# Performance work log

Measured on AMD Instinct MI355X. Metric: run time of the kernel, lower is better.

Reference implementation:

```python
import jax, jax.numpy as jnp
import numpy as np

GROUP_SIZE = 128


def setup_inputs() -> dict:
    key = jax.random.key(0)
    k1, k2, k3 = jax.random.split(key, 3)
    B, S, IN, OUT = 4, 8192, 1024, 1024
    x = jax.random.normal(k1, (B, S, IN), dtype=jnp.float32)
    weight = jax.random.normal(k2, (OUT, IN), dtype=jnp.float32) * 0.02
    bias = jax.random.normal(k3, (OUT,), dtype=jnp.float32) * 0.01
    return {"x": x, "weight": weight, "bias": bias}


def reference(x, weight, bias):
    """Quantized int8 path: quantize() + _forward_int8 of OneBitLinear.

    - weights binarized to +/-1 int8 (sign, with 0 -> -1, matching
      sign().clamp(min=0) bit packing then 2*bit-1)
    - per-group weight scales = group absmax, stored fp16 (as in quantize())
    - activations dynamically quantized per-token to int8
    - int32-accumulated GEMM, rescaled by x_scale * mean group scale per row
    """
    out_f, in_f = weight.shape
    ng = in_f // GROUP_SIZE
    w_g = weight.reshape(out_f, ng, GROUP_SIZE)
    # per-group absmax scales, cast fp16 -> fp32 to mimic fp16 storage
    scales = jnp.maximum(jnp.max(jnp.abs(w_g), axis=-1), 1e-8)
    scales = scales.astype(jnp.float16).astype(jnp.float32)  # [O, ng]
    # +/-1 int8 weights (sign>0 -> +1, else -1; zero maps to -1 like the packer)
    w_int8 = jnp.where(weight > 0, 1, -1).astype(jnp.int8)  # [O, I]

    # dynamic per-token activation quantization
    x_f = x.reshape(-1, in_f)  # [BT, I]
    x_scale = jnp.maximum(jnp.max(jnp.abs(x_f), axis=1, keepdims=True), 1e-8) / 127.0
    x_int8 = jnp.clip(jnp.round(x_f / x_scale), -128, 127).astype(jnp.int8)

    # int8 GEMM with int32 accumulation
    out_i32 = jnp.matmul(
        x_int8.astype(jnp.int32), w_int8.T.astype(jnp.int32)
    )  # [BT, O]

    w_scale_per_row = jnp.mean(scales, axis=1)  # [O]
    out_f32 = out_i32.astype(jnp.float32) * x_scale * w_scale_per_row[None, :]
    out_f32 = out_f32 + bias[None, :]
    return out_f32.reshape(*x.shape[:-1], out_f)
```

## Files before the change

kernel.cpp:

```cpp
#include <hip/hip_runtime.h>
#include <hip/hip_fp16.h>

#define K_DIM 1024
#define N_DIM 1024

typedef int v4i __attribute__((ext_vector_type(4)));

__device__ __forceinline__ void async_load16(const void* g, void* l) {
    __builtin_amdgcn_global_load_lds(
        (const __attribute__((address_space(1))) unsigned int*)g,
        (__attribute__((address_space(3))) unsigned int*)l,
        16, 0, 0);
}

#define BAR() do { asm volatile("" ::: "memory"); \
                   __builtin_amdgcn_s_barrier();  \
                   asm volatile("" ::: "memory"); } while (0)
#define VMCNT0() asm volatile("s_waitcnt vmcnt(0)" ::: "memory")

__global__ __launch_bounds__(256) void prep_w(const float* __restrict__ w,
                                              signed char* __restrict__ wq,
                                              float* __restrict__ wscale) {
    const int lane = threadIdx.x & 63;
    const int row  = blockIdx.x * 4 + (threadIdx.x >> 6);
    const float4* wr = (const float4*)(w + (size_t)row * K_DIM);
    float4 v[4];
#pragma unroll
    for (int j = 0; j < 4; ++j) v[j] = wr[lane * 4 + j];

    float g = 0.f;
#pragma unroll
    for (int j = 0; j < 4; ++j) {
        g = fmaxf(g, fabsf(v[j].x)); g = fmaxf(g, fabsf(v[j].y));
        g = fmaxf(g, fabsf(v[j].z)); g = fmaxf(g, fabsf(v[j].w));
    }
    g = fmaxf(g, __shfl_xor(g, 1, 64));
    g = fmaxf(g, __shfl_xor(g, 2, 64));
    g = fmaxf(g, __shfl_xor(g, 4, 64));
    const float s = __half2float(__float2half(fmaxf(g, 1e-8f)));
    float t = s;
    t += __shfl_xor(t, 8, 64);
    t += __shfl_xor(t, 16, 64);
    t += __shfl_xor(t, 32, 64);
    if (lane == 0) wscale[row] = t * 0.125f;

    int pk[4];
#pragma unroll
    for (int j = 0; j < 4; ++j) {
        const int b0 = (v[j].x > 0.f) ? 1 : -1;
        const int b1 = (v[j].y > 0.f) ? 1 : -1;
        const int b2 = (v[j].z > 0.f) ? 1 : -1;
        const int b3 = (v[j].w > 0.f) ? 1 : -1;
        pk[j] = (b0 & 255) | ((b1 & 255) << 8) | ((b2 & 255) << 16) | (b3 << 24);
    }
    *(int4*)(wq + (size_t)row * K_DIM + lane * 16) = make_int4(pk[0], pk[1], pk[2], pk[3]);
}

__global__ __launch_bounds__(256) void quant_x(const float* __restrict__ x,
                                               signed char* __restrict__ xq,
                                               float* __restrict__ xs) {
    const int lane = threadIdx.x & 63;
    const int row  = blockIdx.x * 4 + (threadIdx.x >> 6);
    const float4* xr = (const float4*)(x + (size_t)row * K_DIM);
    float4 v[4];
#pragma unroll
    for (int j = 0; j < 4; ++j) v[j] = xr[lane * 4 + j];

    float am = 0.f;
#pragma unroll
    for (int j = 0; j < 4; ++j) {
        am = fmaxf(am, fabsf(v[j].x)); am = fmaxf(am, fabsf(v[j].y));
        am = fmaxf(am, fabsf(v[j].z)); am = fmaxf(am, fabsf(v[j].w));
    }
#pragma unroll
    for (int off = 32; off >= 1; off >>= 1) am = fmaxf(am, __shfl_xor(am, off, 64));
    const float scale = fmaxf(am, 1e-8f) / 127.f;
    const float inv   = 1.0f / scale;

    int pk[4];
#pragma unroll
    for (int j = 0; j < 4; ++j) {
        const int b0 = (int)fminf(fmaxf(rintf(v[j].x * inv), -128.f), 127.f);
        const int b1 = (int)fminf(fmaxf(rintf(v[j].y * inv), -128.f), 127.f);
        const int b2 = (int)fminf(fmaxf(rintf(v[j].z * inv), -128.f), 127.f);
        const int b3 = (int)fminf(fmaxf(rintf(v[j].w * inv), -128.f), 127.f);
        pk[j] = (b0 & 255) | ((b1 & 255) << 8) | ((b2 & 255) << 16) | (b3 << 24);
    }
    *(int4*)(xq + (size_t)row * K_DIM + lane * 16) = make_int4(pk[0], pk[1], pk[2], pk[3]);
    if (lane == 0) xs[row] = scale;
}

__global__ __launch_bounds__(512, 2) void gemm_i8(const signed char* __restrict__ A,
                                                  const signed char* __restrict__ Bw,
                                                  const float* __restrict__ xs,
                                                  const float* __restrict__ wscale,
                                                  const float* __restrict__ bias,
                                                  float* __restrict__ out) {
    __shared__ __align__(16) signed char As[2][256 * 64];
    __shared__ __align__(16) signed char Bs[2][256 * 64];

    const int tid  = threadIdx.x;
    const int lane = tid & 63;
    const int wave = tid >> 6;
    const int wm   = wave >> 2;
    const int wn   = wave & 3;

    const int bid  = blockIdx.x;
    const int wgid = (bid & 7) * 64 + (bid >> 3);
    const int mT   = wgid >> 2;
    const int nT   = wgid & 3;
    const size_t mBase = (size_t)mT * 256;
    const int    nBase = nT * 256;

    const int srow = tid >> 2;
    const int skq  = (tid & 3) * 16;
    const signed char* Ag = A  + (mBase + srow) * K_DIM + skq;
    const signed char* Bg = Bw + (size_t)(nBase + srow) * K_DIM + skq;
    const int soff = tid * 16;

#define STAGE(b, kt) do {                                                   \
        const int _ko = (kt) * 64;                                          \
        async_load16(Ag + _ko,                         &As[b][soff]);       \
        async_load16(Ag + (size_t)128 * K_DIM + _ko,   &As[b][8192 + soff]);\
        async_load16(Bg + _ko,                         &Bs[b][soff]);       \
        async_load16(Bg + (size_t)128 * K_DIM + _ko,   &Bs[b][8192 + soff]);\
    } while (0)

    v4i acc[8][4] = {};

    const int r16 = lane & 15;
    const int g16 = (lane >> 4) * 16;
    const int aoff = (wm * 128 + r16) * 64 + g16;
    const int boff = (wn * 64  + r16) * 64 + g16;

    STAGE(0, 0);
    VMCNT0();
    BAR();

    for (int t = 0; t < 16; ++t) {
        const signed char* Ab = As[t & 1];
        const signed char* Bb = Bs[t & 1];

        if (t < 15) STAGE((t + 1) & 1, t + 1);

        v4i af[8], bf[4];
#pragma unroll
        for (int mf = 0; mf < 8; ++mf)
            af[mf] = *(const v4i*)(Ab + aoff + mf * (16 * 64));
#pragma unroll
        for (int nf = 0; nf < 4; ++nf)
            bf[nf] = *(const v4i*)(Bb + boff + nf * (16 * 64));

#pragma unroll
        for (int mf = 0; mf < 8; ++mf)
#pragma unroll
            for (int nf = 0; nf < 4; ++nf)
                acc[mf][nf] = __builtin_amdgcn_mfma_i32_16x16x64_i8(
                    af[mf], bf[nf], acc[mf][nf], 0, 0, 0);

        if (t < 15) {
            __builtin_amdgcn_sched_barrier(0);
            VMCNT0();
            BAR();
        }
    }
#undef STAGE

    const int cc = r16;
    const int rq = (lane >> 4) * 4;
    float xsr[8][4];
#pragma unroll
    for (int mf = 0; mf < 8; ++mf)
#pragma unroll
        for (int i = 0; i < 4; ++i)
            xsr[mf][i] = xs[mBase + wm * 128 + mf * 16 + rq + i];

#pragma unroll
    for (int nf = 0; nf < 4; ++nf) {
        const int col  = nBase + wn * 64 + nf * 16 + cc;
        const float wsc = wscale[col];
        const float bb  = bias[col];
#pragma unroll
        for (int mf = 0; mf < 8; ++mf) {
#pragma unroll
            for (int i = 0; i < 4; ++i) {
                const size_t row = mBase + wm * 128 + mf * 16 + rq + i;
                out[row * N_DIM + col] = (float)acc[mf][nf][i] * xsr[mf][i] * wsc + bb;
            }
        }
    }
}

extern "C" void kernel_launch(void* const* d_in, const int* in_sizes, int n_in,
                              void* d_out, int out_size, void* d_ws, size_t ws_size,
                              hipStream_t stream) {
    const float* x    = (const float*)d_in[0];
    const float* w    = (const float*)d_in[1];
    const float* bias = (const float*)d_in[2];
    float* out = (float*)d_out;

    const int BT = in_sizes[0] / K_DIM;

    char* ws = (char*)d_ws;
    signed char* xq     = (signed char*)ws;
    float*       xs     = (float*)(ws + (size_t)BT * K_DIM);
    signed char* wq     = (signed char*)(ws + (size_t)BT * K_DIM + (size_t)BT * 4);
    float*       wscale = (float*)((char*)wq + (size_t)N_DIM * K_DIM);

    prep_w<<<N_DIM / 4, 256, 0, stream>>>(w, wq, wscale);
    quant_x<<<BT / 4, 256, 0, stream>>>(x, xq, xs);
    gemm_i8<<<(BT / 256) * (N_DIM / 256), 512, 0, stream>>>(xq, wq, xs, wscale, bias, out);
}
```

Measured before the change: 303.5 us.

## Fuse activation quantization into GEMM with full-K int8 A tile in LDS

Removes the separate quant_x kernel. Each GEMM workgroup now quantizes its own 128 rows of x straight into a swizzled 128KB LDS buffer holding the full K extent, then sweeps all four 256-wide N tiles while streaming only B tiles through double-buffered LDS. This drops the int8 activation round trip through global memory and one kernel launch. In exchange it uses 160KB of dynamic LDS, which limits occupancy to one workgroup per CU. The grid shrinks to 256 workgroups, the quantization phase is not overlapped with MFMA work, and B is re-read from L2 by every workgroup.

```diff
diff --git a/kernel.cpp b/kernel.cpp
--- a/kernel.cpp
+++ b/kernel.cpp
@@ -56,136 +56,130 @@
     *(int4*)(wq + (size_t)row * K_DIM + lane * 16) = make_int4(pk[0], pk[1], pk[2], pk[3]);
 }
 
-__global__ __launch_bounds__(256) void quant_x(const float* __restrict__ x,
-                                               signed char* __restrict__ xq,
-                                               float* __restrict__ xs) {
-    const int lane = threadIdx.x & 63;
-    const int row  = blockIdx.x * 4 + (threadIdx.x >> 6);
-    const float4* xr = (const float4*)(x + (size_t)row * K_DIM);
-    float4 v[4];
-#pragma unroll
-    for (int j = 0; j < 4; ++j) v[j] = xr[lane * 4 + j];
-
-    float am = 0.f;
-#pragma unroll
-    for (int j = 0; j < 4; ++j) {
-        am = fmaxf(am, fabsf(v[j].x)); am = fmaxf(am, fabsf(v[j].y));
-        am = fmaxf(am, fabsf(v[j].z)); am = fmaxf(am, fabsf(v[j].w));
-    }
-#pragma unroll
-    for (int off = 32; off >= 1; off >>= 1) am = fmaxf(am, __shfl_xor(am, off, 64));
-    const float scale = fmaxf(am, 1e-8f) / 127.f;
-    const float inv   = 1.0f / scale;
-
-    int pk[4];
-#pragma unroll
-    for (int j = 0; j < 4; ++j) {
-        const int b0 = (int)fminf(fmaxf(rintf(v[j].x * inv), -128.f), 127.f);
-        const int b1 = (int)fminf(fmaxf(rintf(v[j].y * inv), -128.f), 127.f);
-        const int b2 = (int)fminf(fmaxf(rintf(v[j].z * inv), -128.f), 127.f);
-        const int b3 = (int)fminf(fmaxf(rintf(v[j].w * inv), -128.f), 127.f);
-        pk[j] = (b0 & 255) | ((b1 & 255) << 8) | ((b2 & 255) << 16) | (b3 << 24);
-    }
-    *(int4*)(xq + (size_t)row * K_DIM + lane * 16) = make_int4(pk[0], pk[1], pk[2], pk[3]);
-    if (lane == 0) xs[row] = scale;
-}
-
-__global__ __launch_bounds__(512, 2) void gemm_i8(const signed char* __restrict__ A,
-                                                  const signed char* __restrict__ Bw,
-                                                  const float* __restrict__ xs,
-                                                  const float* __restrict__ wscale,
-                                                  const float* __restrict__ bias,
-                                                  float* __restrict__ out) {
-    __shared__ __align__(16) signed char As[2][256 * 64];
-    __shared__ __align__(16) signed char Bs[2][256 * 64];
+__global__ __launch_bounds__(512, 2) void qgemm(const float* __restrict__ x,
+                                                const signed char* __restrict__ Bw,
+                                                const float* __restrict__ wscale,
+                                                const float* __restrict__ bias,
+                                                float* __restrict__ xsg,
+                                                float* __restrict__ out) {
+    extern __shared__ __align__(16) signed char smem[];
+    signed char* As = smem;
+    signed char* Bs = smem + 131072;
 
     const int tid  = threadIdx.x;
     const int lane = tid & 63;
     const int wave = tid >> 6;
-    const int wm   = wave >> 2;
-    const int wn   = wave & 3;
-
-    const int bid  = blockIdx.x;
-    const int wgid = (bid & 7) * 64 + (bid >> 3);
-    const int mT   = wgid >> 2;
-    const int nT   = wgid & 3;
-    const size_t mBase = (size_t)mT * 256;
-    const int    nBase = nT * 256;
+    const size_t mBase = (size_t)blockIdx.x * 128;
+
+    for (int rb = 0; rb < 4; ++rb) {
+        const int r0 = wave * 16 + rb * 4;
+        float4 v[4][4];
+#pragma unroll
+        for (int rr = 0; rr < 4; ++rr) {
+            const float4* xr = (const float4*)(x + (mBase + r0 + rr) * K_DIM);
+#pragma unroll
+            for (int j = 0; j < 4; ++j) v[rr][j] = xr[lane * 4 + j];
+        }
+#pragma unroll
+        for (int rr = 0; rr < 4; ++rr) {
+            const int r = r0 + rr;
+            float am = 0.f;
+#pragma unroll
+            for (int j = 0; j < 4; ++j) {
+                am = fmaxf(am, fabsf(v[rr][j].x)); am = fmaxf(am, fabsf(v[rr][j].y));
+                am = fmaxf(am, fabsf(v[rr][j].z)); am = fmaxf(am, fabsf(v[rr][j].w));
+            }
+#pragma unroll
+            for (int off = 32; off >= 1; off >>= 1) am = fmaxf(am, __shfl_xor(am, off, 64));
+            const float scale = fmaxf(am, 1e-8f) / 127.f;
+            const float inv   = 1.0f / scale;
+            int pk[4];
+#pragma unroll
+            for (int j = 0; j < 4; ++j) {
+                const int b0 = (int)fminf(fmaxf(rintf(v[rr][j].x * inv), -128.f), 127.f);
+                const int b1 = (int)fminf(fmaxf(rintf(v[rr][j].y * inv), -128.f), 127.f);
+                const int b2 = (int)fminf(fmaxf(rintf(v[rr][j].z * inv), -128.f), 127.f);
+                const int b3 = (int)fminf(fmaxf(rintf(v[rr][j].w * inv), -128.f), 127.f);
+                pk[j] = (b0 & 255) | ((b1 & 255) << 8) | ((b2 & 255) << 16) | (b3 << 24);
+            }
+            *(int4*)(As + (size_t)r * 1024 + ((lane ^ (r & 7)) * 16)) =
+                make_int4(pk[0], pk[1], pk[2], pk[3]);
+            if (lane == 0) xsg[mBase + r] = scale;
+        }
+    }
+    __syncthreads();
+
+    const int wm  = wave >> 2;
+    const int wn  = wave & 3;
+    const int r16 = lane & 15;
+    const int g   = lane >> 4;
+
+    const int rq = g * 4;
+    float xsr[4][4];
+#pragma unroll
+    for (int mf = 0; mf < 4; ++mf)
+#pragma unroll
+        for (int i = 0; i < 4; ++i)
+            xsr[mf][i] = __hip_atomic_load(&xsg[mBase + wm * 64 + mf * 16 + rq + i],
+                                           __ATOMIC_RELAXED, __HIP_MEMORY_SCOPE_AGENT);
 
     const int srow = tid >> 2;
     const int skq  = (tid & 3) * 16;
-    const signed char* Ag = A  + (mBase + srow) * K_DIM + skq;
-    const signed char* Bg = Bw + (size_t)(nBase + srow) * K_DIM + skq;
     const int soff = tid * 16;
 
-#define STAGE(b, kt) do {                                                   \
-        const int _ko = (kt) * 64;                                          \
-        async_load16(Ag + _ko,                         &As[b][soff]);       \
-        async_load16(Ag + (size_t)128 * K_DIM + _ko,   &As[b][8192 + soff]);\
-        async_load16(Bg + _ko,                         &Bs[b][soff]);       \
-        async_load16(Bg + (size_t)128 * K_DIM + _ko,   &Bs[b][8192 + soff]);\
-    } while (0)
-
-    v4i acc[8][4] = {};
-
-    const int r16 = lane & 15;
-    const int g16 = (lane >> 4) * 16;
-    const int aoff = (wm * 128 + r16) * 64 + g16;
-    const int boff = (wn * 64  + r16) * 64 + g16;
-
-    STAGE(0, 0);
-    VMCNT0();
-    BAR();
-
-    for (int t = 0; t < 16; ++t) {
-        const signed char* Ab = As[t & 1];
-        const signed char* Bb = Bs[t & 1];
-
-        if (t < 15) STAGE((t + 1) & 1, t + 1);
-
-        v4i af[8], bf[4];
-#pragma unroll
-        for (int mf = 0; mf < 8; ++mf)
-            af[mf] = *(const v4i*)(Ab + aoff + mf * (16 * 64));
-#pragma unroll
-        for (int nf = 0; nf < 4; ++nf)
-            bf[nf] = *(const v4i*)(Bb + boff + nf * (16 * 64));
-
-#pragma unroll
-        for (int mf = 0; mf < 8; ++mf)
+    for (int p = 0; p < 4; ++p) {
+        const int nBase = p * 256;
+        const signed char* Bg = Bw + (size_t)(nBase + srow) * K_DIM + skq;
+
+        v4i acc[4][4] = {};
+
+        async_load16(Bg, Bs + soff);
+        async_load16(Bg + (size_t)128 * K_DIM, Bs + 8192 + soff);
+        VMCNT0();
+        BAR();
+
+        for (int t = 0; t < 16; ++t) {
+            const signed char* Bb = Bs + (t & 1) * 16384;
+            if (t < 15) {
+                const int ko = (t + 1) * 64;
+                signed char* Bn = Bs + ((t + 1) & 1) * 16384;
+                async_load16(Bg + ko, Bn + soff);
+                async_load16(Bg + (size_t)128 * K_DIM + ko, Bn + 8192 + soff);
+            }
+            v4i af[4], bf[4];
+#pragma unroll
+            for (int mf = 0; mf < 4; ++mf) {
+                const int R = wm * 64 + mf * 16 + r16;
+                af[mf] = *(const v4i*)(As + (size_t)R * 1024 + (((t * 4 + g) ^ (R & 7)) * 16));
+            }
 #pragma unroll
             for (int nf = 0; nf < 4; ++nf)
-                acc[mf][nf] = __builtin_amdgcn_mfma_i32_16x16x64_i8(
-                    af[mf], bf[nf], acc[mf][nf], 0, 0, 0);
-
-        if (t < 15) {
-            __builtin_amdgcn_sched_barrier(0);
-            VMCNT0();
-            BAR();
-        }
-    }
-#undef STAGE
-
-    const int cc = r16;
-    const int rq = (lane >> 4) * 4;
-    float xsr[8][4];
-#pragma unroll
-    for (int mf = 0; mf < 8; ++mf)
-#pragma unroll
-        for (int i = 0; i < 4; ++i)
-            xsr[mf][i] = xs[mBase + wm * 128 + mf * 16 + rq + i];
-
-#pragma unroll
-    for (int nf = 0; nf < 4; ++nf) {
-        const int col  = nBase + wn * 64 + nf * 16 + cc;
-        const float wsc = wscale[col];
-        const float bb  = bias[col];
-#pragma unroll
-        for (int mf = 0; mf < 8; ++mf) {
-#pragma unroll
-            for (int i = 0; i < 4; ++i) {
-                const size_t row = mBase + wm * 128 + mf * 16 + rq + i;
-                out[row * N_DIM + col] = (float)acc[mf][nf][i] * xsr[mf][i] * wsc + bb;
+                bf[nf] = *(const v4i*)(Bb + (wn * 64 + nf * 16 + r16) * 64 + g * 16);
+#pragma unroll
+            for (int mf = 0; mf < 4; ++mf)
+#pragma unroll
+                for (int nf = 0; nf < 4; ++nf)
+                    acc[mf][nf] = __builtin_amdgcn_mfma_i32_16x16x64_i8(
+                        af[mf], bf[nf], acc[mf][nf], 0, 0, 0);
+            if (t < 15) {
+                __builtin_amdgcn_sched_barrier(0);
+                VMCNT0();
+                BAR();
+            }
+        }
+
+#pragma unroll
+        for (int nf = 0; nf < 4; ++nf) {
+            const int col   = nBase + wn * 64 + nf * 16 + r16;
+            const float wsc = wscale[col];
+            const float bb  = bias[col];
+#pragma unroll
+            for (int mf = 0; mf < 4; ++mf) {
+#pragma unroll
+                for (int i = 0; i < 4; ++i) {
+                    const size_t row = mBase + wm * 64 + mf * 16 + rq + i;
+                    out[row * N_DIM + col] = (float)acc[mf][nf][i] * xsr[mf][i] * wsc + bb;
+                }
             }
         }
     }
@@ -202,12 +196,17 @@
     const int BT = in_sizes[0] / K_DIM;
 
     char* ws = (char*)d_ws;
-    signed char* xq     = (signed char*)ws;
-    float*       xs     = (float*)(ws + (size_t)BT * K_DIM);
-    signed char* wq     = (signed char*)(ws + (size_t)BT * K_DIM + (size_t)BT * 4);
+    float*       xsg    = (float*)ws;
+    signed char* wq     = (signed char*)(ws + (size_t)BT * 4);
     float*       wscale = (float*)((char*)wq + (size_t)N_DIM * K_DIM);
 
+    static bool s_attr_set = false;
+    if (!s_attr_set) {
+        hipFuncSetAttribute((const void*)qgemm,
+                            hipFuncAttributeMaxDynamicSharedMemorySize, 163840);
+        s_attr_set = true;
+    }
+
     prep_w<<<N_DIM / 4, 256, 0, stream>>>(w, wq, wscale);
-    quant_x<<<BT / 4, 256, 0, stream>>>(x, xq, xs);
-    gemm_i8<<<(BT / 256) * (N_DIM / 256), 512, 0, stream>>>(xq, wq, xs, wscale, bias, out);
-}
+    qgemm<<<BT / 128, 512, 163840, stream>>>(x, wq, wscale, bias, xsg, out);
+}
```

Result: faster. 279.6 us (-7.9%).
